# Kernel tuning notes

Hardware: AMD Instinct MI355X
Metric: run time of the kernel (lower is better)

## Reference

```python
import jax, jax.numpy as jnp
import numpy as np

N = 25000      # number of target nodes
K = 32         # sampled neighbor fanout
F_IN = 256
F_OUT = 256


def setup_inputs() -> dict:
    key = jax.random.key(0)
    k1, k2, k3, k4 = jax.random.split(key, 4)
    x = jax.random.normal(k1, (N, F_IN), dtype=jnp.float32)
    neigh = jax.random.randint(k2, (N, K), 0, N, dtype=jnp.int64)
    # Linear(in_feats, out_feats) parameters
    W = jax.random.normal(k3, (F_IN, F_OUT), dtype=jnp.float32) / np.sqrt(F_IN)
    b = jax.random.normal(k4, (F_OUT,), dtype=jnp.float32) * 0.01
    return {"x": x, "neigh": neigh, "W": W, "b": b}


def reference(x, neigh, W, b):
    # Gather neighbor features: [N, K, F_IN]
    h = x[neigh]
    # Linear + ReLU transform on each neighbor feature
    h = jax.nn.relu(jnp.einsum('nkf,fo->nko', h, W) + b)
    # Element-wise max-pool across the neighbor set -> [N, F_OUT]
    return jnp.max(h, axis=1)
```

## Files before the change

kernel.cpp:

```cpp
#include <hip/hip_runtime.h>
#include <hip/hip_bf16.h>

#define N_NODES 25000
#define KFAN    32
#define FIN     256
#define FOUT    256
#define CHUNK_STRIDE (N_NODES * 64)

typedef float  f32x4  __attribute__((ext_vector_type(4)));
typedef int    i32x4  __attribute__((ext_vector_type(4)));
typedef short  s16x8  __attribute__((ext_vector_type(8)));

__device__ __forceinline__ ushort f2bf(float f) {
    unsigned int u = __float_as_uint(f);
    u += 0x7fffu + ((u >> 16) & 1u);
    return (ushort)(u >> 16);
}
__device__ __forceinline__ unsigned int pack2(float a, float b) {
    return (unsigned int)f2bf(a) | ((unsigned int)f2bf(b) << 16);
}

__global__ __launch_bounds__(256) void transpose_w(
    const float* __restrict__ W, ushort* __restrict__ Wt)
{
    __shared__ float ls[32][33];
    const int bid = blockIdx.x;
    const int kt  = bid & 7;
    const int nt  = bid >> 3;
    const int t   = threadIdx.x;

    {
        int kl = t >> 3, n4 = (t & 7) * 4;
        float4 v = *(const float4*)(W + (size_t)(kt * 32 + kl) * FOUT + nt * 32 + n4);
        ls[kl][n4 + 0] = v.x; ls[kl][n4 + 1] = v.y;
        ls[kl][n4 + 2] = v.z; ls[kl][n4 + 3] = v.w;
    }
    __syncthreads();
    {
        int nl = t >> 3, k4 = (t & 7) * 4;
        ushort4 o;
        o.x = f2bf(ls[k4 + 0][nl]);
        o.y = f2bf(ls[k4 + 1][nl]);
        o.z = f2bf(ls[k4 + 2][nl]);
        o.w = f2bf(ls[k4 + 3][nl]);
        *(ushort4*)(Wt + (size_t)(nt * 32 + nl) * FIN + kt * 32 + k4) = o;
    }
}

__global__ __launch_bounds__(256) void gemm_mfma(
    const float*  __restrict__ x,
    const ushort* __restrict__ Wt,
    const float*  __restrict__ bias,
    ushort*       __restrict__ y)
{
    __shared__ ushort As[64][72];

    const int tid  = threadIdx.x;
    const int lane = tid & 63;
    const int wv   = tid >> 6;
    const int l16  = lane & 15;
    const int q    = lane >> 4;
    const int row0 = blockIdx.x * 64;
    const int n0   = blockIdx.y * 128 + wv * 32;

    f32x4 acc[4][2];
    #pragma unroll
    for (int i = 0; i < 4; ++i)
        #pragma unroll
        for (int j = 0; j < 2; ++j) acc[i][j] = (f32x4)0.f;

    const int r    = tid >> 2;
    const int kcol = (tid & 3) * 16;

    for (int kc = 0; kc < FIN; kc += 64) {
        float4 v0 = make_float4(0.f,0.f,0.f,0.f), v1 = v0, v2 = v0, v3 = v0;
        int gr = row0 + r;
        if (gr < N_NODES) {
            const float* p = x + (size_t)gr * FIN + kc + kcol;
            v0 = *(const float4*)p;
            v1 = *(const float4*)(p + 4);
            v2 = *(const float4*)(p + 8);
            v3 = *(const float4*)(p + 12);
        }
        uint4 pa, pb;
        pa.x = pack2(v0.x, v0.y); pa.y = pack2(v0.z, v0.w);
        pa.z = pack2(v1.x, v1.y); pa.w = pack2(v1.z, v1.w);
        pb.x = pack2(v2.x, v2.y); pb.y = pack2(v2.z, v2.w);
        pb.z = pack2(v3.x, v3.y); pb.w = pack2(v3.z, v3.w);
        *(uint4*)&As[r][kcol]     = pa;
        *(uint4*)&As[r][kcol + 8] = pb;
        __syncthreads();

        #pragma unroll
        for (int kk = 0; kk < 64; kk += 32) {
            const int k0 = kk + q * 8;
            s16x8 a[4], b[2];
            #pragma unroll
            for (int mt = 0; mt < 4; ++mt)
                a[mt] = *(const s16x8*)&As[mt * 16 + l16][k0];
            #pragma unroll
            for (int ct = 0; ct < 2; ++ct)
                b[ct] = *(const s16x8*)(Wt + (size_t)(n0 + ct * 16 + l16) * FIN + kc + k0);
            #pragma unroll
            for (int mt = 0; mt < 4; ++mt)
                #pragma unroll
                for (int ct = 0; ct < 2; ++ct)
                    acc[mt][ct] = __builtin_amdgcn_mfma_f32_16x16x32_bf16(a[mt], b[ct], acc[mt][ct], 0, 0, 0);
        }
        __syncthreads();
    }

    #pragma unroll
    for (int ct = 0; ct < 2; ++ct) {
        const int col = n0 + ct * 16 + l16;
        const float bv = bias[col];
        ushort* yc = y + (size_t)(col >> 6) * CHUNK_STRIDE + (col & 63);
        #pragma unroll
        for (int mt = 0; mt < 4; ++mt) {
            #pragma unroll
            for (int rr = 0; rr < 4; ++rr) {
                int row = row0 + mt * 16 + q * 4 + rr;
                if (row < N_NODES)
                    yc[(size_t)row * 64] = f2bf(fmaxf(acc[mt][ct][rr] + bv, 0.f));
            }
        }
    }
}

__global__ __launch_bounds__(256) void pool_max(
    const ushort* __restrict__ y,
    const int*    __restrict__ neigh,
    float*        __restrict__ out)
{
    const int bid   = blockIdx.x;
    const int chunk = bid & 3;
    const int nb    = bid >> 2;
    const int tid   = threadIdx.x;
    const int lane  = tid & 63;
    const int g     = lane >> 3;
    const int gl    = lane & 7;
    const int wv    = tid >> 6;

    const int n  = nb * 32 + wv * 8 + g;
    const int nc = n < N_NODES ? n : N_NODES - 1;

    const i32x4 iv = __builtin_nontemporal_load(
        (const i32x4*)(neigh + (size_t)nc * KFAN + gl * 4));
    const int base8 = lane & 56;
    int ia[4] = {iv.x, iv.y, iv.z, iv.w};

    int idx[KFAN];
    #pragma unroll
    for (int k = 0; k < KFAN; ++k)
        idx[k] = __shfl(ia[k & 3], base8 + (k >> 2));

    const ushort* yc = y + (size_t)chunk * CHUNK_STRIDE + gl * 8;

    s16x8 acc = (s16x8)0;
    #pragma unroll
    for (int k = 0; k < KFAN; ++k) {
        s16x8 cur = *(const s16x8*)(yc + (size_t)idx[k] * 64);
        acc = __builtin_elementwise_max(acc, cur);
    }

    if (n < N_NODES) {
        f32x4 o0, o1;
        o0.x = __uint_as_float(((unsigned int)(ushort)acc[0]) << 16);
        o0.y = __uint_as_float(((unsigned int)(ushort)acc[1]) << 16);
        o0.z = __uint_as_float(((unsigned int)(ushort)acc[2]) << 16);
        o0.w = __uint_as_float(((unsigned int)(ushort)acc[3]) << 16);
        o1.x = __uint_as_float(((unsigned int)(ushort)acc[4]) << 16);
        o1.y = __uint_as_float(((unsigned int)(ushort)acc[5]) << 16);
        o1.z = __uint_as_float(((unsigned int)(ushort)acc[6]) << 16);
        o1.w = __uint_as_float(((unsigned int)(ushort)acc[7]) << 16);
        float* op = out + (size_t)n * FOUT + chunk * 64 + gl * 8;
        __builtin_nontemporal_store(o0, (f32x4*)op);
        __builtin_nontemporal_store(o1, (f32x4*)(op + 4));
    }
}

extern "C" void kernel_launch(void* const* d_in, const int* in_sizes, int n_in,
                              void* d_out, int out_size, void* d_ws, size_t ws_size,
                              hipStream_t stream) {
    const float* x     = (const float*)d_in[0];
    const int*   neigh = (const int*)  d_in[1];
    const float* W     = (const float*)d_in[2];
    const float* bias  = (const float*)d_in[3];
    float*       out   = (float*)d_out;
    ushort*      y     = (ushort*)d_ws;
    ushort*      Wt    = (ushort*)d_out;

    transpose_w<<<64, 256, 0, stream>>>(W, Wt);

    dim3 g1((N_NODES + 63) / 64, 2);
    gemm_mfma<<<g1, 256, 0, stream>>>(x, Wt, bias, y);

    const int nblocks = ((N_NODES + 31) / 32) * 4;
    pool_max<<<nblocks, 256, 0, stream>>>(y, neigh, out);
}
```

Measured before the change: 120.7 us.

## Assign pool_max work chunks by XCC via atomic tickets for L2 locality

Each pool block reads its hardware XCC id and claims a node-block index from a per-chunk atomic ticket counter, preferring the chunk that matches its XCC. The goal is for each XCC's L2 to hold mostly one 64-column feature chunk of y, cutting cross-XCC duplication and HBM traffic on the random gathers. It adds a memset launch, one atomic per block and a shared-memory broadcast, and relies on blocks being spread across XCCs so that the four chunks divide evenly.

Result: slower. 126.5 us (+4.8%).

```diff
diff --git a/kernel.cpp b/kernel.cpp
--- a/kernel.cpp
+++ b/kernel.cpp
@@ -6,6 +6,7 @@
 #define FIN     256
 #define FOUT    256
 #define CHUNK_STRIDE (N_NODES * 64)
+#define NB_PER_CHUNK 782
 
 typedef float  f32x4  __attribute__((ext_vector_type(4)));
 typedef int    i32x4  __attribute__((ext_vector_type(4)));
@@ -130,12 +131,29 @@
 __global__ __launch_bounds__(256) void pool_max(
     const ushort* __restrict__ y,
     const int*    __restrict__ neigh,
-    float*        __restrict__ out)
+    float*        __restrict__ out,
+    unsigned*     __restrict__ tickets)
 {
-    const int bid   = blockIdx.x;
-    const int chunk = bid & 3;
-    const int nb    = bid >> 2;
-    const int tid   = threadIdx.x;
+    __shared__ int s_chunk, s_nb;
+    const int tid = threadIdx.x;
+
+    if (tid == 0) {
+        unsigned xcc;
+        asm volatile("s_getreg_b32 %0, hwreg(HW_REG_XCC_ID)" : "=s"(xcc));
+        int chunk = -1, nb = 0;
+        for (int a = 0; a < 4; ++a) {
+            int c = ((int)(xcc & 3) + a) & 3;
+            unsigned t = atomicAdd(&tickets[c * 32], 1u);
+            if (t < (unsigned)NB_PER_CHUNK) { chunk = c; nb = (int)t; break; }
+        }
+        s_chunk = chunk;
+        s_nb    = nb;
+    }
+    __syncthreads();
+    const int chunk = s_chunk;
+    const int nb    = s_nb;
+    if (chunk < 0) return;
+
     const int lane  = tid & 63;
     const int g     = lane >> 3;
     const int gl    = lane & 7;
@@ -188,6 +206,7 @@
     const float* bias  = (const float*)d_in[3];
     float*       out   = (float*)d_out;
     ushort*      y     = (ushort*)d_ws;
+    unsigned*    tickets = (unsigned*)((char*)d_ws + (32u << 20));
     ushort*      Wt    = (ushort*)d_out;
 
     transpose_w<<<64, 256, 0, stream>>>(W, Wt);
@@ -195,6 +214,8 @@
     dim3 g1((N_NODES + 63) / 64, 2);
     gemm_mfma<<<g1, 256, 0, stream>>>(x, Wt, bias, y);
 
-    const int nblocks = ((N_NODES + 31) / 32) * 4;
-    pool_max<<<nblocks, 256, 0, stream>>>(y, neigh, out);
-}
+    hipMemsetAsync(tickets, 0, 4 * 32 * sizeof(unsigned), stream);
+
+    const int nblocks = 4 * NB_PER_CHUNK;
+    pool_max<<<nblocks, 256, 0, stream>>>(y, neigh, out, tickets);
+}
```
